# Kernel tuning notes

Hardware: AMD Instinct MI355X
Metric: run time of the kernel (lower is better)

The kernel has to match this reference:

```python
import jax, jax.numpy as jnp
import numpy as np

N_NODES = 32768   # 32 graphs x 1024 points
B_GRAPHS = 32
RATIO = 16
C_IN = 64
HEADS = 4
NEG_SLOPE = 0.2


def setup_inputs() -> dict:
    key = jax.random.key(0)
    ks = jax.random.split(key, 8)
    H, C = HEADS, C_IN
    x = jax.random.normal(ks[0], (N_NODES, C_IN), dtype=jnp.float32)
    edge_index = jax.random.randint(ks[1], (2, 1000), 0, N_NODES)  # ignored by forward
    batch = jnp.repeat(jnp.arange(B_GRAPHS), N_NODES // B_GRAPHS)  # sorted graph ids
    xcent_base = jax.random.normal(ks[2], (RATIO, C_IN), dtype=jnp.float32)
    s = 1.0 / np.sqrt(C_IN)
    W_l = jax.random.normal(ks[3], (C_IN, H * C), dtype=jnp.float32) * s
    b_l = jnp.zeros((H * C,), dtype=jnp.float32)
    W_r = jax.random.normal(ks[4], (C_IN, H * C), dtype=jnp.float32) * s
    b_r = jnp.zeros((H * C,), dtype=jnp.float32)
    att = jax.random.normal(ks[5], (H, C), dtype=jnp.float32) * s
    bias = jnp.zeros((C,), dtype=jnp.float32)
    return {"x": x, "edge_index": edge_index, "batch": batch,
            "xcent_base": xcent_base, "W_l": W_l, "b_l": b_l,
            "W_r": W_r, "b_r": b_r, "att": att, "bias": bias,
            "ratio": RATIO, "batch_size": B_GRAPHS}


def reference(x, edge_index, batch, xcent_base, W_l, b_l, W_r, b_r, att, bias,
              ratio, batch_size):
    # GATv2Conv bipartite: (x_src, x_dst=tiled xcent_base), concat=False (mean over heads)
    H, C = att.shape
    N = x.shape[0]
    T = batch_size * ratio                       # number of target centroids
    # edge list: each source node -> all `ratio` centroids of its graph
    src = jnp.repeat(jnp.arange(N), ratio)       # [E]
    tgt = jnp.tile(jnp.arange(ratio), N) + jnp.repeat(batch, ratio) * ratio  # [E]
    x_dst = jnp.tile(xcent_base, (batch_size, 1))          # [T, C_in]
    x_l = (x @ W_l + b_l).reshape(N, H, C)                 # source transform
    x_r = (x_dst @ W_r + b_r).reshape(T, H, C)             # target transform
    z = x_l[src] + x_r[tgt]                                # [E, H, C]
    z = jnp.where(z >= 0, z, NEG_SLOPE * z)                # LeakyReLU(0.2)
    logit = jnp.einsum('ehc,hc->eh', z, att)               # [E, H]
    # segment softmax over edges sharing a target centroid
    m = jax.ops.segment_max(logit, tgt, num_segments=T)
    ex = jnp.exp(logit - m[tgt])
    den = jax.ops.segment_sum(ex, tgt, num_segments=T)
    alpha = ex / den[tgt]                                  # [E, H]
    out = jax.ops.segment_sum(x_l[src] * alpha[:, :, None], tgt, num_segments=T)
    xcent = out.mean(axis=1) + bias                        # [T, C] (concat=False)
    batchcent = jnp.repeat(jnp.arange(batch_size), ratio)  # [T]
    return xcent, batchcent
```

## Files before the change

### kernel.cpp

```cpp
#include <hip/hip_runtime.h>


typedef __attribute__((ext_vector_type(8))) short short8;
typedef __attribute__((ext_vector_type(4))) float f32x4;

#define NPG 1024
#define NT 512

static __device__ __forceinline__ unsigned short f2bf(float f) {
    unsigned int u = __float_as_uint(f);
    u += 0x7fffu + ((u >> 16) & 1u);
    return (unsigned short)(u >> 16);
}
static __device__ __forceinline__ float bf2f(unsigned short u) {
    return __uint_as_float(((unsigned int)u) << 16);
}
static __device__ __forceinline__ int swz(int row, int unit) { return (unit ^ (row & 7)) << 3; }

__global__ __launch_bounds__(256) void k0_prep(const float* __restrict__ xcb,
                                               const float* __restrict__ W_l,
                                               const float* __restrict__ W_r,
                                               const float* __restrict__ b_r,
                                               const float* __restrict__ att,
                                               float* __restrict__ xrT,
                                               float* __restrict__ xr_att6,
                                               float* __restrict__ att6,
                                               float* __restrict__ att4,
                                               unsigned short* __restrict__ wt,
                                               float* __restrict__ out) {
    int b = blockIdx.x, t = threadIdx.x;
    if (b < 16) {
        int r = b, hc = t;
        float v = b_r[hc];
#pragma unroll
        for (int k = 0; k < 64; ++k)
            v = fmaf(xcb[r * 64 + k], W_r[k * 256 + hc], v);
        xrT[hc * 16 + r] = v;
        float p = 0.6f * att[hc] * v;
        p += __shfl_xor(p, 1);  p += __shfl_xor(p, 2);
        p += __shfl_xor(p, 4);  p += __shfl_xor(p, 8);
        p += __shfl_xor(p, 16); p += __shfl_xor(p, 32);
        if ((t & 63) == 0) xr_att6[r * 4 + (t >> 6)] = p;
    } else {
        att6[t] = 0.6f * att[t];
        att4[t] = 0.4f * att[t];
        unsigned short tmp[64] __attribute__((aligned(16)));
#pragma unroll
        for (int k = 0; k < 64; ++k) tmp[k] = f2bf(W_l[k * 256 + t]);
#pragma unroll
        for (int q = 0; q < 8; ++q)
            *(short8*)(wt + t * 64 + q * 8) = *(const short8*)(tmp + q * 8);
        out[NT * 64 + t]       = (float)(t >> 4);
        out[NT * 64 + 256 + t] = (float)((256 + t) >> 4);
    }
}

__global__ __launch_bounds__(512, 4) void k1_fused(const float* __restrict__ x,
                                                   const unsigned short* __restrict__ wt,
                                                   const float* __restrict__ b_l,
                                                   const float* __restrict__ att6,
                                                   const float* __restrict__ att4,
                                                   const float* __restrict__ xrT,
                                                   const float* __restrict__ xr_att6,
                                                   unsigned short* __restrict__ ws_pvh,
                                                   float* __restrict__ ws_denp) {
    __shared__ __align__(16) short LL[320][64];
    short (*X)[64] = LL;
    short (*E)[64] = LL + 256;

    const int t = threadIdx.x;
    const int blk = blockIdx.x;
    const int n0 = blk * 64;

    {
        int n = t >> 3, u = t & 7;
        const float* p = x + (size_t)(n0 + n) * 64 + u * 8;
        float4 v0 = *(const float4*)p;
        float4 v1 = *(const float4*)(p + 4);
        unsigned short h8[8] __attribute__((aligned(16)));
        h8[0]=f2bf(v0.x); h8[1]=f2bf(v0.y); h8[2]=f2bf(v0.z); h8[3]=f2bf(v0.w);
        h8[4]=f2bf(v1.x); h8[5]=f2bf(v1.y); h8[6]=f2bf(v1.z); h8[7]=f2bf(v1.w);
        *(short8*)(&X[n][swz(n, u)]) = *(const short8*)h8;
    }
    __syncthreads();

    const int l = t & 63;
    const int w = t >> 6;
    const int h    = __builtin_amdgcn_readfirstlane(w & 3);
    const int half = __builtin_amdgcn_readfirstlane(w >> 2);
    const int lm = l & 15, lq = l >> 4;

    short8 af[2][2], bfr[4][2];
#pragma unroll
    for (int mt = 0; mt < 2; ++mt)
#pragma unroll
        for (int ks = 0; ks < 2; ++ks) {
            int row = half * 32 + mt * 16 + lm;
            af[mt][ks] = *(const short8*)(&X[row][swz(row, ks * 4 + lq)]);
        }
#pragma unroll
    for (int nt = 0; nt < 4; ++nt)
#pragma unroll
        for (int ks = 0; ks < 2; ++ks)
            bfr[nt][ks] = *(const short8*)(wt + (size_t)(h * 64 + nt * 16 + lm) * 64 + ks * 32 + lq * 8);

    f32x4 acc[2][4];
#pragma unroll
    for (int mt = 0; mt < 2; ++mt)
#pragma unroll
        for (int nt = 0; nt < 4; ++nt) { f32x4 z = {0.f,0.f,0.f,0.f}; acc[mt][nt] = z; }
#pragma unroll
    for (int mt = 0; mt < 2; ++mt)
#pragma unroll
        for (int nt = 0; nt < 4; ++nt)
#pragma unroll
            for (int ks = 0; ks < 2; ++ks)
                acc[mt][nt] = __builtin_amdgcn_mfma_f32_16x16x32_bf16(
                    af[mt][ks], bfr[nt][ks], acc[mt][nt], 0, 0, 0);

    __syncthreads();

#pragma unroll
    for (int nt = 0; nt < 4; ++nt) {
        float bl = b_l[h * 64 + nt * 16 + lm];
#pragma unroll
        for (int mt = 0; mt < 2; ++mt) {
            unsigned int d0 = (unsigned int)f2bf(acc[mt][nt][0] + bl) |
                              ((unsigned int)f2bf(acc[mt][nt][1] + bl) << 16);
            unsigned int d1 = (unsigned int)f2bf(acc[mt][nt][2] + bl) |
                              ((unsigned int)f2bf(acc[mt][nt][3] + bl) << 16);
            int row = h * 64 + nt * 16 + lm;
            int ncol = half * 32 + mt * 16 + lq * 4;
            int col = swz(row, ncol >> 3) + (ncol & 7);
            *(uint2*)(&X[row][col]) = make_uint2(d0, d1);
        }
    }
    __syncthreads();

    float base = 0.f;
    float lacc[8];
#pragma unroll
    for (int rr = 0; rr < 8; ++rr) lacc[rr] = 0.f;
#pragma unroll 4
    for (int c = 0; c < 64; ++c) {
        int row = h * 64 + c;
        float xv = bf2f((unsigned short)X[row][swz(row, l >> 3) + (l & 7)]);
        base = fmaf(xv, att6[row], base);
        float a4 = att4[row];
        const float* xp = xrT + (size_t)row * 16 + half * 8;
#pragma unroll
        for (int rr = 0; rr < 8; ++rr)
            lacc[rr] = fmaf(fabsf(xv + xp[rr]), a4, lacc[rr]);
    }
#pragma unroll
    for (int rr = 0; rr < 8; ++rr) {
        int r = half * 8 + rr;
        float ex = __expf(base + lacc[rr] + xr_att6[r * 4 + h]);
        int erow = h * 16 + r;
        E[erow][swz(erow, l >> 3) + (l & 7)] = (short)f2bf(ex);
    }
    __syncthreads();

    short8 ap[2];
#pragma unroll
    for (int ks = 0; ks < 2; ++ks) {
        int erow = h * 16 + lm;
        ap[ks] = *(const short8*)(&E[erow][swz(erow, ks * 4 + lq)]);
    }
    f32x4 pacc[2], dacc;
    { f32x4 z = {0.f,0.f,0.f,0.f}; pacc[0]=z; pacc[1]=z; dacc=z; }
#pragma unroll
    for (int ks = 0; ks < 2; ++ks) {
#pragma unroll
        for (int ntl = 0; ntl < 2; ++ntl) {
            int row = h * 64 + (half * 2 + ntl) * 16 + lm;
            short8 bp = *(const short8*)(&X[row][swz(row, ks * 4 + lq)]);
            pacc[ntl] = __builtin_amdgcn_mfma_f32_16x16x32_bf16(ap[ks], bp, pacc[ntl], 0, 0, 0);
        }
        if (half == 0) {
            short o = (lm == 0) ? (short)0x3F80 : (short)0;
            short8 onesf = {o, o, o, o, o, o, o, o};
            dacc = __builtin_amdgcn_mfma_f32_16x16x32_bf16(ap[ks], onesf, dacc, 0, 0, 0);
        }
    }

    unsigned short* pvb = ws_pvh + ((size_t)blk * 4 + h) * 1024;
#pragma unroll
    for (int ntl = 0; ntl < 2; ++ntl)
#pragma unroll
        for (int j = 0; j < 4; ++j)
            pvb[(lq * 4 + j) * 64 + (half * 2 + ntl) * 16 + lm] = f2bf(pacc[ntl][j]);
    if (half == 0 && lm == 0) {
#pragma unroll
        for (int j = 0; j < 4; ++j)
            ws_denp[((size_t)blk * 4 + h) * 16 + lq * 4 + j] = dacc[j];
    }
}

__global__ __launch_bounds__(256) void k2_final(const unsigned short* __restrict__ ws_pvh,
                                                const float* __restrict__ ws_denp,
                                                const float* __restrict__ bias,
                                                float* __restrict__ out) {
    int b = blockIdx.x;
    int g = b >> 2;
    int r = (b & 3) * 4 + (threadIdx.x >> 6);
    int c = threadIdx.x & 63;
    float acc = 0.f;
#pragma unroll
    for (int h = 0; h < 4; ++h) {
        float num = 0.f, den = 0.f;
#pragma unroll
        for (int tl = 0; tl < 16; ++tl) {
            num += bf2f(ws_pvh[(((size_t)(g * 16 + tl)) * 4 + h) * 1024 + r * 64 + c]);
            den += ws_denp[((size_t)(g * 16 + tl) * 4 + h) * 16 + r];
        }
        acc += num / den;
    }
    out[(size_t)(g * 16 + r) * 64 + c] = fmaf(0.25f, acc, bias[c]);
}

extern "C" void kernel_launch(void* const* d_in, const int* in_sizes, int n_in,
                              void* d_out, int out_size, void* d_ws, size_t ws_size,
                              hipStream_t stream) {
    const float* x    = (const float*)d_in[0];
    const float* xcb  = (const float*)d_in[3];
    const float* W_l  = (const float*)d_in[4];
    const float* b_l  = (const float*)d_in[5];
    const float* W_r  = (const float*)d_in[6];
    const float* b_r  = (const float*)d_in[7];
    const float* att  = (const float*)d_in[8];
    const float* bias = (const float*)d_in[9];
    float* out = (float*)d_out;

    unsigned short* ws_pvh = (unsigned short*)d_ws;
    float* ws_denp = (float*)(ws_pvh + 2097152);
    float* xrT     = ws_denp + 32768;
    float* xr_att6 = xrT + 4096;
    float* att6    = xr_att6 + 64;
    float* att4    = att6 + 256;
    unsigned short* wt = (unsigned short*)(att4 + 256);

    k0_prep<<<17, 256, 0, stream>>>(xcb, W_l, W_r, b_r, att, xrT, xr_att6, att6, att4, wt, out);
    k1_fused<<<512, 512, 0, stream>>>(x, wt, b_l, att6, att4, xrT, xr_att6, ws_pvh, ws_denp);
    k2_final<<<128, 256, 0, stream>>>(ws_pvh, ws_denp, bias, out);
}
```

Measured before the change: 32.65 us.

## Halve k1 block to 256 threads, stage xrT in LDS, use packed bf16 convert

New measurement: 32.24 us. Within noise of the previous version (-1.3%).

```diff
diff --git a/kernel.cpp b/kernel.cpp
--- a/kernel.cpp
+++ b/kernel.cpp
@@ -7,10 +7,15 @@
 #define NPG 1024
 #define NT 512
 
+static __device__ __forceinline__ unsigned int cvt2(float lo, float hi) {
+    unsigned int r;
+    asm("v_cvt_pk_bf16_f32 %0, %1, %2" : "=v"(r) : "v"(lo), "v"(hi));
+    return r;
+}
 static __device__ __forceinline__ unsigned short f2bf(float f) {
-    unsigned int u = __float_as_uint(f);
-    u += 0x7fffu + ((u >> 16) & 1u);
-    return (unsigned short)(u >> 16);
+    unsigned int r;
+    asm("v_cvt_pk_bf16_f32 %0, %1, %1" : "=v"(r) : "v"(f));
+    return (unsigned short)r;
 }
 static __device__ __forceinline__ float bf2f(unsigned short u) {
     return __uint_as_float(((unsigned int)u) << 16);
@@ -44,18 +49,19 @@
     } else {
         att6[t] = 0.6f * att[t];
         att4[t] = 0.4f * att[t];
-        unsigned short tmp[64] __attribute__((aligned(16)));
-#pragma unroll
-        for (int k = 0; k < 64; ++k) tmp[k] = f2bf(W_l[k * 256 + t]);
+        unsigned int tmp[32] __attribute__((aligned(16)));
+#pragma unroll
+        for (int k = 0; k < 32; ++k)
+            tmp[k] = cvt2(W_l[(2 * k) * 256 + t], W_l[(2 * k + 1) * 256 + t]);
 #pragma unroll
         for (int q = 0; q < 8; ++q)
-            *(short8*)(wt + t * 64 + q * 8) = *(const short8*)(tmp + q * 8);
+            *(uint4*)(wt + t * 64 + q * 8) = *(const uint4*)(tmp + q * 4);
         out[NT * 64 + t]       = (float)(t >> 4);
         out[NT * 64 + 256 + t] = (float)((256 + t) >> 4);
     }
 }
 
-__global__ __launch_bounds__(512, 4) void k1_fused(const float* __restrict__ x,
+__global__ __launch_bounds__(256, 2) void k1_fused(const float* __restrict__ x,
                                                    const unsigned short* __restrict__ wt,
                                                    const float* __restrict__ b_l,
                                                    const float* __restrict__ att6,
@@ -65,6 +71,7 @@
                                                    unsigned short* __restrict__ ws_pvh,
                                                    float* __restrict__ ws_denp) {
     __shared__ __align__(16) short LL[320][64];
+    __shared__ __align__(16) float XR4[256][16];
     short (*X)[64] = LL;
     short (*E)[64] = LL + 256;
 
@@ -73,29 +80,36 @@
     const int n0 = blk * 64;
 
     {
-        int n = t >> 3, u = t & 7;
-        const float* p = x + (size_t)(n0 + n) * 64 + u * 8;
+        int n = t >> 2, u0 = (t & 3) * 2;
+        const float* p = x + (size_t)(n0 + n) * 64 + u0 * 8;
         float4 v0 = *(const float4*)p;
         float4 v1 = *(const float4*)(p + 4);
-        unsigned short h8[8] __attribute__((aligned(16)));
-        h8[0]=f2bf(v0.x); h8[1]=f2bf(v0.y); h8[2]=f2bf(v0.z); h8[3]=f2bf(v0.w);
-        h8[4]=f2bf(v1.x); h8[5]=f2bf(v1.y); h8[6]=f2bf(v1.z); h8[7]=f2bf(v1.w);
-        *(short8*)(&X[n][swz(n, u)]) = *(const short8*)h8;
+        float4 v2 = *(const float4*)(p + 8);
+        float4 v3 = *(const float4*)(p + 12);
+        uint4 a, b;
+        a.x = cvt2(v0.x, v0.y); a.y = cvt2(v0.z, v0.w);
+        a.z = cvt2(v1.x, v1.y); a.w = cvt2(v1.z, v1.w);
+        b.x = cvt2(v2.x, v2.y); b.y = cvt2(v2.z, v2.w);
+        b.z = cvt2(v3.x, v3.y); b.w = cvt2(v3.z, v3.w);
+        *(uint4*)(&X[n][swz(n, u0)])     = a;
+        *(uint4*)(&X[n][swz(n, u0 + 1)]) = b;
+        const float4* xr = (const float4*)(xrT + t * 16);
+        float4 r0 = xr[0], r1 = xr[1], r2 = xr[2], r3 = xr[3];
+        float4* xd = (float4*)(&XR4[t][0]);
+        xd[0] = r0; xd[1] = r1; xd[2] = r2; xd[3] = r3;
     }
     __syncthreads();
 
     const int l = t & 63;
-    const int w = t >> 6;
-    const int h    = __builtin_amdgcn_readfirstlane(w & 3);
-    const int half = __builtin_amdgcn_readfirstlane(w >> 2);
+    const int h = __builtin_amdgcn_readfirstlane(t >> 6);
     const int lm = l & 15, lq = l >> 4;
 
-    short8 af[2][2], bfr[4][2];
-#pragma unroll
-    for (int mt = 0; mt < 2; ++mt)
+    short8 af[4][2], bfr[4][2];
+#pragma unroll
+    for (int mt = 0; mt < 4; ++mt)
 #pragma unroll
         for (int ks = 0; ks < 2; ++ks) {
-            int row = half * 32 + mt * 16 + lm;
+            int row = mt * 16 + lm;
             af[mt][ks] = *(const short8*)(&X[row][swz(row, ks * 4 + lq)]);
         }
 #pragma unroll
@@ -104,13 +118,13 @@
         for (int ks = 0; ks < 2; ++ks)
             bfr[nt][ks] = *(const short8*)(wt + (size_t)(h * 64 + nt * 16 + lm) * 64 + ks * 32 + lq * 8);
 
-    f32x4 acc[2][4];
-#pragma unroll
-    for (int mt = 0; mt < 2; ++mt)
+    f32x4 acc[4][4];
+#pragma unroll
+    for (int mt = 0; mt < 4; ++mt)
 #pragma unroll
         for (int nt = 0; nt < 4; ++nt) { f32x4 z = {0.f,0.f,0.f,0.f}; acc[mt][nt] = z; }
 #pragma unroll
-    for (int mt = 0; mt < 2; ++mt)
+    for (int mt = 0; mt < 4; ++mt)
 #pragma unroll
         for (int nt = 0; nt < 4; ++nt)
 #pragma unroll
@@ -124,13 +138,11 @@
     for (int nt = 0; nt < 4; ++nt) {
         float bl = b_l[h * 64 + nt * 16 + lm];
 #pragma unroll
-        for (int mt = 0; mt < 2; ++mt) {
-            unsigned int d0 = (unsigned int)f2bf(acc[mt][nt][0] + bl) |
-                              ((unsigned int)f2bf(acc[mt][nt][1] + bl) << 16);
-            unsigned int d1 = (unsigned int)f2bf(acc[mt][nt][2] + bl) |
-                              ((unsigned int)f2bf(acc[mt][nt][3] + bl) << 16);
+        for (int mt = 0; mt < 4; ++mt) {
+            unsigned int d0 = cvt2(acc[mt][nt][0] + bl, acc[mt][nt][1] + bl);
+            unsigned int d1 = cvt2(acc[mt][nt][2] + bl, acc[mt][nt][3] + bl);
             int row = h * 64 + nt * 16 + lm;
-            int ncol = half * 32 + mt * 16 + lq * 4;
+            int ncol = mt * 16 + lq * 4;
             int col = swz(row, ncol >> 3) + (ncol & 7);
             *(uint2*)(&X[row][col]) = make_uint2(d0, d1);
         }
@@ -138,24 +150,28 @@
     __syncthreads();
 
     float base = 0.f;
-    float lacc[8];
-#pragma unroll
-    for (int rr = 0; rr < 8; ++rr) lacc[rr] = 0.f;
+    float lacc[16];
+#pragma unroll
+    for (int r = 0; r < 16; ++r) lacc[r] = 0.f;
 #pragma unroll 4
     for (int c = 0; c < 64; ++c) {
         int row = h * 64 + c;
         float xv = bf2f((unsigned short)X[row][swz(row, l >> 3) + (l & 7)]);
         base = fmaf(xv, att6[row], base);
         float a4 = att4[row];
-        const float* xp = xrT + (size_t)row * 16 + half * 8;
-#pragma unroll
-        for (int rr = 0; rr < 8; ++rr)
-            lacc[rr] = fmaf(fabsf(xv + xp[rr]), a4, lacc[rr]);
-    }
-#pragma unroll
-    for (int rr = 0; rr < 8; ++rr) {
-        int r = half * 8 + rr;
-        float ex = __expf(base + lacc[rr] + xr_att6[r * 4 + h]);
+        float xr4v[16];
+        const float4* xp = (const float4*)(&XR4[row][0]);
+        *(float4*)(xr4v + 0)  = xp[0];
+        *(float4*)(xr4v + 4)  = xp[1];
+        *(float4*)(xr4v + 8)  = xp[2];
+        *(float4*)(xr4v + 12) = xp[3];
+#pragma unroll
+        for (int r = 0; r < 16; ++r)
+            lacc[r] = fmaf(fabsf(xv + xr4v[r]), a4, lacc[r]);
+    }
+#pragma unroll
+    for (int r = 0; r < 16; ++r) {
+        float ex = __expf(base + lacc[r] + xr_att6[r * 4 + h]);
         int erow = h * 16 + r;
         E[erow][swz(erow, l >> 3) + (l & 7)] = (short)f2bf(ex);
     }
@@ -167,30 +183,29 @@
         int erow = h * 16 + lm;
         ap[ks] = *(const short8*)(&E[erow][swz(erow, ks * 4 + lq)]);
     }
-    f32x4 pacc[2], dacc;
-    { f32x4 z = {0.f,0.f,0.f,0.f}; pacc[0]=z; pacc[1]=z; dacc=z; }
+    short o = (lm == 0) ? (short)0x3F80 : (short)0;
+    short8 onesf = {o, o, o, o, o, o, o, o};
+
+    f32x4 pacc[4], dacc;
+    { f32x4 z = {0.f,0.f,0.f,0.f}; pacc[0]=z; pacc[1]=z; pacc[2]=z; pacc[3]=z; dacc=z; }
 #pragma unroll
     for (int ks = 0; ks < 2; ++ks) {
 #pragma unroll
-        for (int ntl = 0; ntl < 2; ++ntl) {
-            int row = h * 64 + (half * 2 + ntl) * 16 + lm;
+        for (int nt = 0; nt < 4; ++nt) {
+            int row = h * 64 + nt * 16 + lm;
             short8 bp = *(const short8*)(&X[row][swz(row, ks * 4 + lq)]);
-            pacc[ntl] = __builtin_amdgcn_mfma_f32_16x16x32_bf16(ap[ks], bp, pacc[ntl], 0, 0, 0);
-        }
-        if (half == 0) {
-            short o = (lm == 0) ? (short)0x3F80 : (short)0;
-            short8 onesf = {o, o, o, o, o, o, o, o};
-            dacc = __builtin_amdgcn_mfma_f32_16x16x32_bf16(ap[ks], onesf, dacc, 0, 0, 0);
-        }
+            pacc[nt] = __builtin_amdgcn_mfma_f32_16x16x32_bf16(ap[ks], bp, pacc[nt], 0, 0, 0);
+        }
+        dacc = __builtin_amdgcn_mfma_f32_16x16x32_bf16(ap[ks], onesf, dacc, 0, 0, 0);
     }
 
     unsigned short* pvb = ws_pvh + ((size_t)blk * 4 + h) * 1024;
 #pragma unroll
-    for (int ntl = 0; ntl < 2; ++ntl)
+    for (int nt = 0; nt < 4; ++nt)
 #pragma unroll
         for (int j = 0; j < 4; ++j)
-            pvb[(lq * 4 + j) * 64 + (half * 2 + ntl) * 16 + lm] = f2bf(pacc[ntl][j]);
-    if (half == 0 && lm == 0) {
+            pvb[(lq * 4 + j) * 64 + nt * 16 + lm] = f2bf(pacc[nt][j]);
+    if (lm == 0) {
 #pragma unroll
         for (int j = 0; j < 4; ++j)
             ws_denp[((size_t)blk * 4 + h) * 16 + lq * 4 + j] = dacc[j];
@@ -241,6 +256,6 @@
     unsigned short* wt = (unsigned short*)(att4 + 256);
 
     k0_prep<<<17, 256, 0, stream>>>(xcb, W_l, W_r, b_r, att, xrT, xr_att6, att6, att4, wt, out);
-    k1_fused<<<512, 512, 0, stream>>>(x, wt, b_l, att6, att4, xrT, xr_att6, ws_pvh, ws_denp);
+    k1_fused<<<512, 256, 0, stream>>>(x, wt, b_l, att6, att4, xrT, xr_att6, ws_pvh, ws_denp);
     k2_final<<<128, 256, 0, stream>>>(ws_pvh, ws_denp, bias, out);
 }
```
